# Kernel optimization log

Hardware: AMD Instinct MI355X
Metric: run time of the kernel (lower is better)

## Reference

```python
import jax, jax.numpy as jnp
import numpy as np

N = 100000          # nodes
E = 1600000         # edges (avg degree 16)
D_IN = 128
D_OUT = 32
K_HOPS = 10         # Taylor truncation order used by TDConv


def setup_inputs() -> dict:
    key = jax.random.key(0)
    k1, k2, k3 = jax.random.split(key, 3)
    x = jax.random.normal(k1, (N, D_IN), dtype=jnp.float32)
    edge_index = jax.random.randint(k2, (2, E), 0, N, dtype=jnp.int64)
    W = jax.random.normal(k3, (D_IN, D_OUT), dtype=jnp.float32) * (1.0 / np.sqrt(D_IN))
    b = jnp.zeros((D_OUT,), dtype=jnp.float32)
    t = jnp.asarray(5.0, dtype=jnp.float32)  # learnable diffusion time, init_t
    return {"x": x, "edge_index": edge_index, "W": W, "b": b, "t": t}


def reference(x, edge_index, W, b, t):
    n = x.shape[0]
    # Linear projection
    h = x @ W + b  # [N, D_OUT]

    # GCN normalization with self-loops: A_hat = D^{-1/2} (A + I) D^{-1/2}
    self_loop = jnp.arange(n, dtype=edge_index.dtype)
    src = jnp.concatenate([edge_index[0], self_loop])
    dst = jnp.concatenate([edge_index[1], self_loop])
    deg = jax.ops.segment_sum(jnp.ones(src.shape[0], h.dtype), dst, num_segments=n)
    dinv = jnp.where(deg > 0, jax.lax.rsqrt(deg), 0.0)
    norm = (dinv[src] * dinv[dst])[:, None]  # [E+N, 1]

    # Truncated heat-kernel Taylor diffusion: sum_k e^{-t} t^k/k! * A_hat^k h
    coeff = jnp.exp(-t)          # k = 0 coefficient
    out = coeff * h
    cur = h
    for k in range(1, K_HOPS + 1):
        cur = jax.ops.segment_sum(cur[src] * norm, dst, num_segments=n)  # A_hat @ cur
        coeff = coeff * t / k    # e^{-t} t^k / k!
        out = out + coeff * cur
    return out
```

## Files before the change

kernel.cpp:

```cpp
#include <hip/hip_runtime.h>
#include <hip/hip_bf16.h>

#define K_HOPS 10
#define D_IN   128
#define D_OUT  32

__global__ void detect_coeffs_kernel(const void* __restrict__ edges,
                                     const float* __restrict__ t_ptr,
                                     float* __restrict__ coeffs,
                                     int* __restrict__ flag64) {
    if (blockIdx.x == 0 && threadIdx.x == 0) {
        const int* e32 = (const int*)edges;
        int is64 = 1;
        for (int i = 1; i < 128; i += 2) {
            if (e32[i] != 0) { is64 = 0; break; }
        }
        *flag64 = is64;
        float t = *t_ptr;
        float c = expf(-t);
        coeffs[0] = c;
        for (int k = 1; k <= K_HOPS; ++k) {
            c = c * t / (float)k;
            coeffs[k] = c;
        }
    }
}

__device__ __forceinline__ int ld_idx(const void* p, long long i, int is64) {
    return is64 ? (int)((const long long*)p)[i] : ((const int*)p)[i];
}

__global__ void degree_kernel(const void* __restrict__ edges, long long E,
                              int* __restrict__ degcnt,
                              const int* __restrict__ flag64) {
    int is64 = *flag64;
    long long i = (long long)blockIdx.x * blockDim.x + threadIdx.x;
    if (i < E) {
        int d = ld_idx(edges, E + i, is64);
        atomicAdd(&degcnt[d], 1);
    }
}

__global__ void dinv_kernel(const int* __restrict__ degcnt,
                            float* __restrict__ dinv, int N) {
    int i = blockIdx.x * blockDim.x + threadIdx.x;
    if (i < N) {
        dinv[i] = rsqrtf((float)(degcnt[i] + 1));
    }
}

__global__ void __launch_bounds__(256)
scan_sums_kernel(const int* __restrict__ degcnt, int* __restrict__ blocksums,
                 int N) {
    __shared__ int red[256];
    int tid = threadIdx.x;
    int i0 = blockIdx.x * 1024 + tid * 4;
    int s = 0;
    if (i0 + 3 < N) {
        int4 v = *(const int4*)(degcnt + i0);
        s = v.x + v.y + v.z + v.w;
    } else {
#pragma unroll
        for (int j = 0; j < 4; ++j) {
            int i = i0 + j;
            if (i < N) s += degcnt[i];
        }
    }
    red[tid] = s;
    __syncthreads();
    for (int off = 128; off > 0; off >>= 1) {
        if (tid < off) red[tid] += red[tid + off];
        __syncthreads();
    }
    if (tid == 0) blocksums[blockIdx.x] = red[0];
}

__global__ void __launch_bounds__(1024)
scan_offsets_kernel(const int* __restrict__ blocksums,
                    int* __restrict__ blockoffs, int* __restrict__ row_ptr,
                    int nblocks, int N) {
    __shared__ int sh[1024];
    int tid = threadIdx.x;
    sh[tid] = (tid < nblocks) ? blocksums[tid] : 0;
    __syncthreads();
    for (int off = 1; off < 1024; off <<= 1) {
        int u = (tid >= off) ? sh[tid - off] : 0;
        __syncthreads();
        sh[tid] += u;
        __syncthreads();
    }
    if (tid < nblocks) blockoffs[tid] = (tid == 0) ? 0 : sh[tid - 1];
    if (tid == 0) row_ptr[N] = sh[nblocks - 1];
}

__global__ void __launch_bounds__(256)
scan_write_kernel(const int* __restrict__ degcnt,
                  const int* __restrict__ blockoffs,
                  int* __restrict__ row_ptr, int N) {
    __shared__ int red[256];
    int tid = threadIdx.x;
    int i0 = blockIdx.x * 1024 + tid * 4;
    int a0 = 0, a1 = 0, a2 = 0, a3 = 0;
    if (i0 + 3 < N) {
        int4 v = *(const int4*)(degcnt + i0);
        a0 = v.x; a1 = v.y; a2 = v.z; a3 = v.w;
    } else {
        if (i0     < N) a0 = degcnt[i0];
        if (i0 + 1 < N) a1 = degcnt[i0 + 1];
        if (i0 + 2 < N) a2 = degcnt[i0 + 2];
        if (i0 + 3 < N) a3 = degcnt[i0 + 3];
    }
    red[tid] = a0 + a1 + a2 + a3;
    __syncthreads();
    for (int off = 1; off < 256; off <<= 1) {
        int u = (tid >= off) ? red[tid - off] : 0;
        __syncthreads();
        red[tid] += u;
        __syncthreads();
    }
    int pre = blockoffs[blockIdx.x] + ((tid == 0) ? 0 : red[tid - 1]);
    int p0 = pre, p1 = p0 + a0, p2 = p1 + a1, p3 = p2 + a2;
    if (i0 + 3 < N) {
        *(int4*)(row_ptr + i0) = make_int4(p0, p1, p2, p3);
    } else {
        if (i0     < N) row_ptr[i0]     = p0;
        if (i0 + 1 < N) row_ptr[i0 + 1] = p1;
        if (i0 + 2 < N) row_ptr[i0 + 2] = p2;
        if (i0 + 3 < N) row_ptr[i0 + 3] = p3;
    }
}

__global__ void scatter_kernel(const void* __restrict__ edges, long long E,
                               const int* __restrict__ row_ptr,
                               int* __restrict__ fill,
                               int* __restrict__ csr,
                               const int* __restrict__ flag64) {
    int is64 = *flag64;
    long long i = (long long)blockIdx.x * blockDim.x + threadIdx.x;
    if (i < E) {
        int s = ld_idx(edges, i, is64);
        int d = ld_idx(edges, E + i, is64);
        int pos = atomicAdd(&fill[d], 1);
        __builtin_nontemporal_store(s, &csr[row_ptr[d] + pos]);
    }
}

#define NB 64
__global__ void __launch_bounds__(256)
proj_kernel(const float* __restrict__ x, const float* __restrict__ W,
            const float* __restrict__ b, const float* __restrict__ coeffs,
            const float* __restrict__ dinv,
            float* __restrict__ y0, float* __restrict__ out, int N) {
    __shared__ float Wl[D_IN * D_OUT];
    __shared__ float bl[D_OUT];
    __shared__ float xl[NB * (D_IN + 1)];

    int tid = threadIdx.x;
    for (int i = tid; i < D_IN * D_OUT; i += 256) Wl[i] = W[i];
    if (tid < D_OUT) bl[tid] = b[tid];

    int n0 = blockIdx.x * NB;
    for (int v = tid; v < NB * D_IN / 4; v += 256) {
        int flat = v * 4;
        long long gflat = (long long)n0 * D_IN + flat;
        float4 val = make_float4(0.f, 0.f, 0.f, 0.f);
        if (gflat + 3 < (long long)N * D_IN) {
            val = *(const float4*)(x + gflat);
        }
        int node = flat >> 7;
        int j    = flat & 127;
        float* p = &xl[node * (D_IN + 1) + j];
        p[0] = val.x; p[1] = val.y; p[2] = val.z; p[3] = val.w;
    }
    __syncthreads();

    int node_l = tid >> 2;
    int gnode  = n0 + node_l;
    int f0     = (tid & 3) * 8;
    float acc[8];
#pragma unroll
    for (int ff = 0; ff < 8; ++ff) acc[ff] = 0.f;

    if (gnode < N) {
        const float* xr = &xl[node_l * (D_IN + 1)];
        for (int j = 0; j < D_IN; ++j) {
            float xv = xr[j];
#pragma unroll
            for (int ff = 0; ff < 8; ++ff) {
                acc[ff] += xv * Wl[j * D_OUT + f0 + ff];
            }
        }
        float c0 = coeffs[0];
        float dv = dinv[gnode];
        size_t base = (size_t)gnode * D_OUT + f0;
#pragma unroll
        for (int ff = 0; ff < 8; ++ff) {
            float yv = dv * (acc[ff] + bl[f0 + ff]);
            y0[base + ff]  = yv;
            out[base + ff] = c0 * yv;
        }
    }
}

__global__ void __launch_bounds__(256)
hop_kernel(const float* __restrict__ cur, float* __restrict__ nxt,
           float* __restrict__ out,
           const int* __restrict__ csr, const int* __restrict__ row_ptr,
           const float* __restrict__ dinv, const float* __restrict__ coeffs,
           int k, int N) {
    int gtid = blockIdx.x * blockDim.x + threadIdx.x;
    int node = gtid >> 3;
    int g    = gtid & 7;
    if (node >= N) return;

    int start = row_ptr[node];
    int len   = row_ptr[node + 1] - start;

    const float4* curv = (const float4*)cur;
    float ax = 0.f, ay = 0.f, az = 0.f, aw = 0.f;
    for (int base = 0; base < len; base += 8) {
        int rem = len - base;
        int cnt = rem < 8 ? rem : 8;
        int meta = csr[start + base + (g < cnt ? g : cnt - 1)];
#pragma unroll
        for (int j = 0; j < 8; ++j) {
            int s = __shfl(meta, j, 8);
            float4 v = curv[(s << 3) + g];
            if (j < cnt) { ax += v.x; ay += v.y; az += v.z; aw += v.w; }
        }
    }
    float4 sv = curv[(node << 3) + g];
    ax += sv.x; ay += sv.y; az += sv.z; aw += sv.w;

    float dv = dinv[node];
    float s2 = dv * dv;
    float4 y = make_float4(ax * s2, ay * s2, az * s2, aw * s2);

    int o = (node << 3) + g;
    ((float4*)nxt)[o] = y;
    float c = coeffs[k];
    float4 ov = ((float4*)out)[o];
    ov.x += c * y.x; ov.y += c * y.y; ov.z += c * y.z; ov.w += c * y.w;
    ((float4*)out)[o] = ov;
}

__global__ void final_scale_kernel(float* __restrict__ out,
                                   const int* __restrict__ degcnt, int N) {
    int i = blockIdx.x * blockDim.x + threadIdx.x;
    int n4 = N * (D_OUT / 4);
    if (i < n4) {
        int node = i >> 3;
        float sc = sqrtf((float)(degcnt[node] + 1));
        float4 v = ((float4*)out)[i];
        v.x *= sc; v.y *= sc; v.z *= sc; v.w *= sc;
        ((float4*)out)[i] = v;
    }
}

extern "C" void kernel_launch(void* const* d_in, const int* in_sizes, int n_in,
                              void* d_out, int out_size, void* d_ws, size_t ws_size,
                              hipStream_t stream) {
    const float* x     = (const float*)d_in[0];
    const void*  edges = d_in[1];
    const float* W     = (const float*)d_in[2];
    const float* b     = (const float*)d_in[3];
    const float* t     = (const float*)d_in[4];
    float*       out   = (float*)d_out;

    long long E = in_sizes[1] / 2;
    int       N = in_sizes[0] / D_IN;
    int nblocks = (N + 1023) / 1024;

    char*  ws  = (char*)d_ws;
    size_t off = 0;
    auto alloc = [&](size_t bytes) -> void* {
        void* p = ws + off;
        off = (off + bytes + 255) & ~(size_t)255;
        return p;
    };
    float* coeffs    = (float*)alloc(64);
    int*   flag64    = (int*)alloc(4);
    int*   degcnt    = (int*)alloc((size_t)N * 8);
    int*   fill      = degcnt + N;
    float* dinv      = (float*)alloc((size_t)N * 4);
    int*   row_ptr   = (int*)alloc(((size_t)N + 1) * 4);
    int*   blocksums = (int*)alloc((size_t)nblocks * 4);
    int*   blockoffs = (int*)alloc((size_t)nblocks * 4);
    int*   csr       = (int*)alloc((size_t)E * 4);
    float* buf0      = (float*)alloc((size_t)N * D_OUT * 4);
    float* buf1      = (float*)alloc((size_t)N * D_OUT * 4);
    (void)ws_size;

    detect_coeffs_kernel<<<1, 64, 0, stream>>>(edges, t, coeffs, flag64);
    hipMemsetAsync(degcnt, 0, (size_t)N * 8, stream);

    int egrid = (int)((E + 255) / 256);
    degree_kernel<<<egrid, 256, 0, stream>>>(edges, E, degcnt, flag64);
    dinv_kernel<<<(N + 255) / 256, 256, 0, stream>>>(degcnt, dinv, N);

    scan_sums_kernel<<<nblocks, 256, 0, stream>>>(degcnt, blocksums, N);
    scan_offsets_kernel<<<1, 1024, 0, stream>>>(blocksums, blockoffs, row_ptr,
                                                nblocks, N);
    scan_write_kernel<<<nblocks, 256, 0, stream>>>(degcnt, blockoffs, row_ptr, N);

    scatter_kernel<<<egrid, 256, 0, stream>>>(edges, E, row_ptr, fill, csr,
                                              flag64);
    proj_kernel<<<(N + NB - 1) / NB, 256, 0, stream>>>(x, W, b, coeffs, dinv,
                                                       buf0, out, N);

    float* bufs[2] = {buf0, buf1};
    int hgrid = (int)(((long long)N * 8 + 255) / 256);
    for (int k = 1; k <= K_HOPS; ++k) {
        hop_kernel<<<hgrid, 256, 0, stream>>>(bufs[(k - 1) & 1], bufs[k & 1], out,
                                              csr, row_ptr, dinv, coeffs, k, N);
    }
    final_scale_kernel<<<(N * (D_OUT / 4) + 255) / 256, 256, 0, stream>>>(
        out, degcnt, N);
}
```

Before: 666.6 us.

## Partition CSR scatter by destination range and fuse final scale into last hop

The scatter kernel now splits into 8 partitions by destination node range. Each group of blocks runs a grid-stride loop over all edges and handles only the edges whose destination falls in its range, so atomics and CSR writes stay within a smaller region of memory, which is meant to improve L2 locality. Each partition has to re-read the destination indices, so that stream is read 8 times. The sqrt-degree final scaling is also folded into the last hop kernel, which drops one kernel launch and one full read-write pass over the output.

```diff
diff --git a/kernel.cpp b/kernel.cpp
--- a/kernel.cpp
+++ b/kernel.cpp
@@ -130,18 +130,25 @@
     }
 }
 
-__global__ void scatter_kernel(const void* __restrict__ edges, long long E,
-                               const int* __restrict__ row_ptr,
-                               int* __restrict__ fill,
-                               int* __restrict__ csr,
-                               const int* __restrict__ flag64) {
+__global__ void __launch_bounds__(256)
+scatter_kernel(const void* __restrict__ edges, long long E,
+               const int* __restrict__ row_ptr,
+               int* __restrict__ fill,
+               int* __restrict__ csr,
+               const int* __restrict__ flag64, int shift) {
     int is64 = *flag64;
-    long long i = (long long)blockIdx.x * blockDim.x + threadIdx.x;
-    if (i < E) {
-        int s = ld_idx(edges, i, is64);
+    int part    = blockIdx.x & 7;
+    int pbid    = blockIdx.x >> 3;
+    int pblocks = gridDim.x >> 3;
+    long long stride = (long long)pblocks * blockDim.x;
+    for (long long i = (long long)pbid * blockDim.x + threadIdx.x; i < E;
+         i += stride) {
         int d = ld_idx(edges, E + i, is64);
-        int pos = atomicAdd(&fill[d], 1);
-        __builtin_nontemporal_store(s, &csr[row_ptr[d] + pos]);
+        if ((d >> shift) == part) {
+            int s = ld_idx(edges, i, is64);
+            int pos = atomicAdd(&fill[d], 1);
+            csr[row_ptr[d] + pos] = s;
+        }
     }
 }
 
@@ -207,7 +214,7 @@
            float* __restrict__ out,
            const int* __restrict__ csr, const int* __restrict__ row_ptr,
            const float* __restrict__ dinv, const float* __restrict__ coeffs,
-           int k, int N) {
+           const int* __restrict__ degcnt, int k, int N) {
     int gtid = blockIdx.x * blockDim.x + threadIdx.x;
     int node = gtid >> 3;
     int g    = gtid & 7;
@@ -241,20 +248,11 @@
     float c = coeffs[k];
     float4 ov = ((float4*)out)[o];
     ov.x += c * y.x; ov.y += c * y.y; ov.z += c * y.z; ov.w += c * y.w;
+    if (k == K_HOPS) {
+        float sc = sqrtf((float)(degcnt[node] + 1));
+        ov.x *= sc; ov.y *= sc; ov.z *= sc; ov.w *= sc;
+    }
     ((float4*)out)[o] = ov;
-}
-
-__global__ void final_scale_kernel(float* __restrict__ out,
-                                   const int* __restrict__ degcnt, int N) {
-    int i = blockIdx.x * blockDim.x + threadIdx.x;
-    int n4 = N * (D_OUT / 4);
-    if (i < n4) {
-        int node = i >> 3;
-        float sc = sqrtf((float)(degcnt[node] + 1));
-        float4 v = ((float4*)out)[i];
-        v.x *= sc; v.y *= sc; v.z *= sc; v.w *= sc;
-        ((float4*)out)[i] = v;
-    }
 }
 
 extern "C" void kernel_launch(void* const* d_in, const int* in_sizes, int n_in,
@@ -270,6 +268,9 @@
     long long E = in_sizes[1] / 2;
     int       N = in_sizes[0] / D_IN;
     int nblocks = (N + 1023) / 1024;
+
+    int shift = 1;
+    while ((((long long)N - 1) >> shift) > 7) shift++;
 
     char*  ws  = (char*)d_ws;
     size_t off = 0;
@@ -303,8 +304,9 @@
                                                 nblocks, N);
     scan_write_kernel<<<nblocks, 256, 0, stream>>>(degcnt, blockoffs, row_ptr, N);
 
-    scatter_kernel<<<egrid, 256, 0, stream>>>(edges, E, row_ptr, fill, csr,
-                                              flag64);
+    scatter_kernel<<<8 * 768, 256, 0, stream>>>(edges, E, row_ptr, fill, csr,
+                                                flag64, shift);
+
     proj_kernel<<<(N + NB - 1) / NB, 256, 0, stream>>>(x, W, b, coeffs, dinv,
                                                        buf0, out, N);
 
@@ -312,8 +314,7 @@
     int hgrid = (int)(((long long)N * 8 + 255) / 256);
     for (int k = 1; k <= K_HOPS; ++k) {
         hop_kernel<<<hgrid, 256, 0, stream>>>(bufs[(k - 1) & 1], bufs[k & 1], out,
-                                              csr, row_ptr, dinv, coeffs, k, N);
-    }
-    final_scale_kernel<<<(N * (D_OUT / 4) + 255) / 256, 256, 0, stream>>>(
-        out, degcnt, N);
-}
+                                              csr, row_ptr, dinv, coeffs,
+                                              degcnt, k, N);
+    }
+}
```

Result: faster. 625.9 us (-6.1%).
